# Optimization experiments

Measured on AMD Instinct MI355X. Metric: run time of the kernel, lower is better.

## Reference

```python
import jax, jax.numpy as jnp
import numpy as np

D = 64
H = 8


def setup_inputs() -> dict:
    key = jax.random.key(0)
    ks = jax.random.split(key, 6)
    b, l = 2, 4096
    scale = 1.0 / np.sqrt(D)
    x = jax.random.normal(ks[0], (b, l, D), dtype=jnp.float32)
    Wq = jax.random.normal(ks[1], (D, D * H), dtype=jnp.float32) * scale
    Wk = jax.random.normal(ks[2], (D, D * H), dtype=jnp.float32) * scale
    Wv = jax.random.normal(ks[3], (D, D * H), dtype=jnp.float32) * scale
    Wu = jax.random.normal(ks[4], (H * D, D), dtype=jnp.float32) * (1.0 / np.sqrt(H * D))
    bu = jax.random.normal(ks[5], (D,), dtype=jnp.float32) * 0.01
    return {"x": x, "Wq": Wq, "Wk": Wk, "Wv": Wv, "Wu": Wu, "bu": bu}


def reference(x, Wq, Wk, Wv, Wu, bu):
    b, l, d = x.shape
    h = H
    # per-head projections: each head uses FULL width d (as in the torch module)
    q = jnp.einsum('bld,de->ble', x, Wq).reshape(b, l, h, d)
    k = jnp.einsum('bld,de->ble', x, Wk).reshape(b, l, h, d)
    v = jnp.einsum('bld,de->ble', x, Wv).reshape(b, l, h, d)
    # scores [b,h,l,l] scaled by 1/sqrt(d)
    scores = jnp.einsum('blhd,bmhd->bhlm', q, k) / jnp.sqrt(jnp.asarray(d, x.dtype))
    w = jax.nn.softmax(scores, axis=-1)
    out = jnp.einsum('bhlm,bmhd->blhd', w, v).reshape(b, l, h * d)
    return out @ Wu + bu
```

## Files before the change

### kernel.cpp

```cpp
#include <hip/hip_runtime.h>
#include <hip/hip_bf16.h>
#include <stdint.h>

typedef float    f32x16 __attribute__((ext_vector_type(16)));
typedef float    f32x4  __attribute__((ext_vector_type(4)));
typedef __bf16   bf16x8 __attribute__((ext_vector_type(8)));
typedef uint32_t u32x4  __attribute__((ext_vector_type(4)));

#define WS_QG    0
#define WS_KG    8388608
#define WS_VTG   16777216
#define WS_ATTN  25165824
#define WS_WT    33554432
#define WS_WUT   33751040

__device__ __forceinline__ f32x16 zero16(){
  f32x16 z;
  #pragma unroll
  for (int i = 0; i < 16; ++i) z[i] = 0.0f;
  return z;
}

__device__ __forceinline__ uint16_t bf16b(float v){
  return __builtin_bit_cast(uint16_t, __float2bfloat16(v));
}

__device__ __forceinline__ uint32_t pk2(float a, float b){
  return (uint32_t)bf16b(a) | ((uint32_t)bf16b(b) << 16);
}

__device__ __forceinline__ void plswap(uint32_t &a, uint32_t &b){
  asm volatile("v_permlane32_swap_b32 %0, %1" : "+v"(a), "+v"(b));
}

__device__ __forceinline__ float sum16(const f32x16& s){
  float a0 = (s[0]+s[1]) + (s[2]+s[3]),   a1 = (s[4]+s[5]) + (s[6]+s[7]);
  float a2 = (s[8]+s[9]) + (s[10]+s[11]), a3 = (s[12]+s[13]) + (s[14]+s[15]);
  return (a0 + a1) + (a2 + a3);
}

__device__ __forceinline__ void bar_ws(){
  asm volatile("s_waitcnt lgkmcnt(0)" ::: "memory");
  __builtin_amdgcn_s_barrier();
  asm volatile("" ::: "memory");
}

__global__ void prep_w(const float* __restrict__ Wq, const float* __restrict__ Wk,
                       const float* __restrict__ Wv, const float* __restrict__ Wu,
                       char* __restrict__ ws){
  int tid = blockIdx.x * 256 + threadIdx.x;
  if (tid < 3*32768){
    int which = tid >> 15;
    int idx   = tid & 32767;
    int e = idx & 511, k = idx >> 9;
    const float* W = (which == 0) ? Wq : (which == 1 ? Wk : Wv);
    float v = W[k*512 + e];
    if (which == 0) v *= 0.18033688011112042f;
    ((uint16_t*)(ws + WS_WT))[which*32768 + e*64 + k] = bf16b(v);
  } else {
    int idx = tid - 3*32768;
    int c = idx & 63, e = idx >> 6;
    ((uint16_t*)(ws + WS_WUT))[c*512 + e] = bf16b(Wu[e*64 + c]);
  }
}

__global__ __launch_bounds__(256,2) void qkv_proj(const float* __restrict__ x,
                                                  char* __restrict__ ws){
  const int lane = threadIdx.x & 63;
  const int widx = threadIdx.x >> 6;
  const int x8 = blockIdx.x & 7;
  const int o  = blockIdx.x >> 3;
  const int rt = x8*32 + o/6;
  const int rem = (o%6)*4 + widx;
  const int mm = rem >> 3, cb = rem & 7;
  const int col  = lane & 31, hi = lane >> 5;

  __shared__ __align__(16) uint16_t tbuf[4][64*40];

  const uint16_t* Wt = (const uint16_t*)(ws + WS_WT) + mm*32768;

  bf16x8 af[4];
  {
    const float* xr = x + (size_t)(rt*32 + col)*64 + hi*8;
    #pragma unroll
    for (int ks = 0; ks < 4; ++ks){
      float4 a0 = *(const float4*)(xr + ks*16);
      float4 a1 = *(const float4*)(xr + ks*16 + 4);
      uint4 u;
      u.x = pk2(a0.x, a0.y); u.y = pk2(a0.z, a0.w);
      u.z = pk2(a1.x, a1.y); u.w = pk2(a1.z, a1.w);
      af[ks] = __builtin_bit_cast(bf16x8, u);
    }
  }

  f32x16 acc0 = zero16(), acc1 = zero16();
  {
    const uint16_t* w0p = Wt + (size_t)(cb*64 + col)*64 + hi*8;
    const uint16_t* w1p = w0p + 32*64;
    #pragma unroll
    for (int ks = 0; ks < 4; ++ks){
      bf16x8 b0 = *(const bf16x8*)(w0p + ks*16);
      bf16x8 b1 = *(const bf16x8*)(w1p + ks*16);
      acc0 = __builtin_amdgcn_mfma_f32_32x32x16_bf16(af[ks], b0, acc0, 0, 0, 0);
      acc1 = __builtin_amdgcn_mfma_f32_32x32x16_bf16(af[ks], b1, acc1, 0, 0, 0);
    }
  }

  uint16_t* Qg  = (uint16_t*)(ws + WS_QG);
  uint16_t* Kg  = (uint16_t*)(ws + WS_KG);
  uint16_t* Vtg = (uint16_t*)(ws + WS_VTG);
  if (mm == 2){
    uint16_t* tb = tbuf[widx];
    #pragma unroll
    for (int r = 0; r < 16; ++r){
      int tok = (r&3) + 8*(r>>2) + 4*hi;
      tb[col*40 + tok]        = bf16b(acc0[r]);
      tb[(col+32)*40 + tok]   = bf16b(acc1[r]);
    }
    int b    = (rt*32) >> 12;
    int ltok = (rt*32) & 4095;
    const int vrow = lane >> 2, ch = lane & 3;
    #pragma unroll
    for (int o2 = 0; o2 < 4; ++o2){
      int dv = o2*16 + vrow;
      uint4 u = *(const uint4*)(tb + dv*40 + ch*8);
      *(uint4*)(Vtg + ((size_t)((b*8 + cb)*64 + dv))*4096 + ltok + ch*8) = u;
    }
  } else {
    uint16_t* G = mm ? Kg : Qg;
    #pragma unroll
    for (int r = 0; r < 16; ++r){
      int row  = rt*32 + (r&3) + 8*(r>>2) + 4*hi;
      int b    = row >> 12, ltok = row & 4095;
      size_t base = (size_t)((b*8 + cb)*4096 + ltok)*64;
      G[base + col]      = bf16b(acc0[r]);
      G[base + col + 32] = bf16b(acc1[r]);
    }
  }
}

__global__ __launch_bounds__(256,1) void attn_fa(char* __restrict__ ws){
  const int lane = threadIdx.x & 63;
  const int wave = threadIdx.x >> 6;
  const int u   = blockIdx.x >> 3;
  const int bh  = (blockIdx.x & 7) + ((u >> 4) << 3);
  const int qt  = u & 15;
  const int col = lane & 31, hi = lane >> 5;
  const int kxor = (col & 7) << 4;

  const uint16_t* Qg  = (const uint16_t*)(ws + WS_QG)  + (size_t)bh*262144;
  const uint16_t* Kg  = (const uint16_t*)(ws + WS_KG)  + (size_t)bh*262144;
  const uint16_t* Vtg = (const uint16_t*)(ws + WS_VTG) + (size_t)bh*262144;
  uint16_t* attn = (uint16_t*)(ws + WS_ATTN);

  __shared__ __align__(16) char smem[33792];
  char* buf0 = smem;
  char* buf1 = smem + 16384;

  const int qbase = qt*256 + wave*64;

  bf16x8 qf0[4], qf1[4];
  {
    const uint16_t* qr0 = Qg + (size_t)(qbase + col)*64 + hi*8;
    const uint16_t* qr1 = qr0 + 32*64;
    #pragma unroll
    for (int ds = 0; ds < 4; ++ds){
      qf0[ds] = *(const bf16x8*)(qr0 + ds*16);
      qf1[ds] = *(const bf16x8*)(qr1 + ds*16);
    }
  }

  const int rr = lane >> 3, ch = lane & 7;
  const int kRow0 = wave*16 + rr;
  const uint16_t* kSrc = Kg  + (size_t)kRow0*64   + ch*8;
  const uint16_t* vSrc = Vtg + (size_t)kRow0*4096 + ch*8;
  const int sDst = kRow0*128 + ((ch*16) ^ (rr << 4));

  f32x16 ot00 = zero16(), ot01 = zero16(), ot10 = zero16(), ot11 = zero16();
  float rs0 = 0.0f, rs1 = 0.0f;

  u32x4 rK0, rK1, rV0, rV1;
  auto loadKV = [&](int t){
    const uint16_t* ks = kSrc + (size_t)t*4096;
    const uint16_t* vs = vSrc + t*64;
    rK0 = *(const u32x4*)(ks);
    rK1 = *(const u32x4*)(ks + 512);
    rV0 = *(const u32x4*)(vs);
    rV1 = *(const u32x4*)(vs + (size_t)8*4096);
  };
  auto writeKV = [&](char* buf){
    *(u32x4*)(buf + sDst)           = rK0;
    *(u32x4*)(buf + sDst + 1024)    = rK1;
    *(u32x4*)(buf + 8192 + sDst)        = rV0;
    *(u32x4*)(buf + 8192 + sDst + 1024) = rV1;
  };

  auto pack2 = [&](const f32x16& s, bf16x8& f0, bf16x8& f1){
    uint32_t w0 = pk2(s[0],  s[1]),  w1 = pk2(s[2],  s[3]);
    uint32_t w2 = pk2(s[4],  s[5]),  w3 = pk2(s[6],  s[7]);
    uint32_t w4 = pk2(s[8],  s[9]),  w5 = pk2(s[10], s[11]);
    uint32_t w6 = pk2(s[12], s[13]), w7 = pk2(s[14], s[15]);
    plswap(w0, w2); plswap(w1, w3); plswap(w4, w6); plswap(w5, w7);
    u32x4 u0; u0.x = w0; u0.y = w1; u0.z = w2; u0.w = w3;
    u32x4 u1; u1.x = w4; u1.y = w5; u1.z = w6; u1.w = w7;
    f0 = __builtin_bit_cast(bf16x8, u0);
    f1 = __builtin_bit_cast(bf16x8, u1);
  };

  auto compute = [&](const char* buf){
    const char* kb = buf;
    const char* vb = buf + 8192;
    bf16x8 pA[4], pB[4];
    #pragma unroll
    for (int ks2 = 0; ks2 < 2; ++ks2){
      f32x16 sA = zero16(), sB = zero16();
      __builtin_amdgcn_s_setprio(1);
      #pragma unroll
      for (int ds = 0; ds < 4; ++ds){
        bf16x8 kf = *(const bf16x8*)(kb + (ks2*32 + col)*128 + ((ds*32 + hi*16) ^ kxor));
        sA = __builtin_amdgcn_mfma_f32_32x32x16_bf16(kf, qf0[ds], sA, 0, 0, 0);
        sB = __builtin_amdgcn_mfma_f32_32x32x16_bf16(kf, qf1[ds], sB, 0, 0, 0);
      }
      __builtin_amdgcn_s_setprio(0);
      #pragma unroll
      for (int r = 0; r < 16; ++r) sA[r] = __builtin_amdgcn_exp2f(sA[r]);
      #pragma unroll
      for (int r = 0; r < 16; ++r) sB[r] = __builtin_amdgcn_exp2f(sB[r]);
      rs0 += sum16(sA);
      rs1 += sum16(sB);
      pack2(sA, pA[ks2*2], pA[ks2*2+1]);
      pack2(sB, pB[ks2*2], pB[ks2*2+1]);
    }
    __builtin_amdgcn_s_setprio(1);
    #pragma unroll
    for (int sl = 0; sl < 4; ++sl){
      bf16x8 vf0 = *(const bf16x8*)(vb + col*128 + ((sl*32 + hi*16) ^ kxor));
      ot00 = __builtin_amdgcn_mfma_f32_32x32x16_bf16(vf0, pA[sl], ot00, 0, 0, 0);
      ot01 = __builtin_amdgcn_mfma_f32_32x32x16_bf16(vf0, pB[sl], ot01, 0, 0, 0);
      bf16x8 vf1 = *(const bf16x8*)(vb + (32 + col)*128 + ((sl*32 + hi*16) ^ kxor));
      ot10 = __builtin_amdgcn_mfma_f32_32x32x16_bf16(vf1, pA[sl], ot10, 0, 0, 0);
      ot11 = __builtin_amdgcn_mfma_f32_32x32x16_bf16(vf1, pB[sl], ot11, 0, 0, 0);
    }
    __builtin_amdgcn_s_setprio(0);
  };

  loadKV(0);
  writeKV(buf0);
  loadKV(1);
  bar_ws();

  for (int t = 0; t < 64; ++t){
    char* cur = (t & 1) ? buf1 : buf0;
    char* nxt = (t & 1) ? buf0 : buf1;
    writeKV(nxt);
    loadKV((t+2 < 64) ? t+2 : 63);
    compute(cur);
    bar_ws();
  }

  rs0 += __shfl_xor(rs0, 32);
  rs1 += __shfl_xor(rs1, 32);
  float inv0 = 1.0f / rs0, inv1 = 1.0f / rs1;

  uint32_t* ow = (uint32_t*)(smem + wave*8448);
  #pragma unroll
  for (int od = 0; od < 2; ++od){
    #pragma unroll
    for (int j = 0; j < 8; ++j){
      int p = (j&1) + 4*(j>>1) + 2*hi + 16*od;
      const f32x16& a0 = od ? ot10 : ot00;
      const f32x16& a1 = od ? ot11 : ot01;
      ow[(col     )*33 + p] = pk2(a0[2*j]*inv0, a0[2*j+1]*inv0);
      ow[(col + 32)*33 + p] = pk2(a1[2*j]*inv1, a1[2*j+1]*inv1);
    }
  }
  {
    #pragma unroll
    for (int oo = 0; oo < 8; ++oo){
      int q = oo*8 + rr;
      u32x4 uu = *(const u32x4*)(ow + q*33 + ch*4);
      size_t row = (size_t)((bh >> 3)*4096 + qbase + q);
      *(u32x4*)(attn + row*512 + (bh & 7)*64 + ch*8) = uu;
    }
  }
}

__global__ __launch_bounds__(256) void out_proj(const char* __restrict__ ws,
                                                const float* __restrict__ bu,
                                                float* __restrict__ out){
  const int lane = threadIdx.x & 63;
  const int wave = blockIdx.x*4 + (threadIdx.x >> 6);
  const int mt = wave >> 2, cb = wave & 3;
  const int rc = lane & 15, kg = lane >> 4;

  const uint16_t* attn = (const uint16_t*)(ws + WS_ATTN);
  const uint16_t* Wut  = (const uint16_t*)(ws + WS_WUT);

  const uint16_t* ar = attn + (size_t)(mt*16 + rc)*512 + kg*8;
  const uint16_t* bp = Wut  + (size_t)(cb*16 + rc)*512 + kg*8;

  f32x4 acc = {0.0f, 0.0f, 0.0f, 0.0f};
  #pragma unroll
  for (int ks = 0; ks < 16; ++ks){
    bf16x8 af = *(const bf16x8*)(ar + ks*32);
    bf16x8 bf = *(const bf16x8*)(bp + ks*32);
    acc = __builtin_amdgcn_mfma_f32_16x16x32_bf16(af, bf, acc, 0, 0, 0);
  }
  float bias = bu[cb*16 + rc];
  #pragma unroll
  for (int r = 0; r < 4; ++r){
    int orow = mt*16 + kg*4 + r;
    out[(size_t)orow*64 + cb*16 + rc] = acc[r] + bias;
  }
}

extern "C" void kernel_launch(void* const* d_in, const int* in_sizes, int n_in,
                              void* d_out, int out_size, void* d_ws, size_t ws_size,
                              hipStream_t stream){
  const float* x  = (const float*)d_in[0];
  const float* Wq = (const float*)d_in[1];
  const float* Wk = (const float*)d_in[2];
  const float* Wv = (const float*)d_in[3];
  const float* Wu = (const float*)d_in[4];
  const float* bu = (const float*)d_in[5];
  char*  ws  = (char*)d_ws;
  float* out = (float*)d_out;

  prep_w  <<<dim3(512),  dim3(256), 0, stream>>>(Wq, Wk, Wv, Wu, ws);
  qkv_proj<<<dim3(1536), dim3(256), 0, stream>>>(x, ws);
  attn_fa <<<dim3(256),  dim3(256), 0, stream>>>(ws);
  out_proj<<<dim3(512),  dim3(256), 0, stream>>>(ws, bu, out);
}
```

Measured before the change: 197.4 us.

## Split attention KV range across wave pairs and stage Q/K stores through LDS

The attention kernel now launches twice as many blocks with 128 query rows each. The four waves split into two query halves times two KV halves, and the partial outputs and row sums are merged through shared memory before normalization. This is meant to raise occupancy and CU coverage (512 blocks, launch bounds 2) and to halve the serial KV loop per wave. The cost is doubled LDS per block and an extra reduction step. Separately, Q/K writes in the projection kernel are transposed through LDS so they become coalesced 16-byte stores instead of scattered 2-byte stores.

Measured after the change: 178.9 us. -9.3%, faster.

```diff
diff --git a/kernel.cpp b/kernel.cpp
--- a/kernel.cpp
+++ b/kernel.cpp
@@ -75,7 +75,7 @@
   const int mm = rem >> 3, cb = rem & 7;
   const int col  = lane & 31, hi = lane >> 5;
 
-  __shared__ __align__(16) uint16_t tbuf[4][64*40];
+  __shared__ __align__(16) uint16_t tbuf[4][2560];
 
   const uint16_t* Wt = (const uint16_t*)(ws + WS_WT) + mm*32768;
 
@@ -109,42 +109,49 @@
   uint16_t* Qg  = (uint16_t*)(ws + WS_QG);
   uint16_t* Kg  = (uint16_t*)(ws + WS_KG);
   uint16_t* Vtg = (uint16_t*)(ws + WS_VTG);
+  uint16_t* tb  = tbuf[widx];
+  const int b     = (rt*32) >> 12;
+  const int ltok0 = (rt*32) & 4095;
   if (mm == 2){
-    uint16_t* tb = tbuf[widx];
     #pragma unroll
     for (int r = 0; r < 16; ++r){
       int tok = (r&3) + 8*(r>>2) + 4*hi;
       tb[col*40 + tok]        = bf16b(acc0[r]);
       tb[(col+32)*40 + tok]   = bf16b(acc1[r]);
     }
-    int b    = (rt*32) >> 12;
-    int ltok = (rt*32) & 4095;
     const int vrow = lane >> 2, ch = lane & 3;
     #pragma unroll
     for (int o2 = 0; o2 < 4; ++o2){
       int dv = o2*16 + vrow;
-      uint4 u = *(const uint4*)(tb + dv*40 + ch*8);
-      *(uint4*)(Vtg + ((size_t)((b*8 + cb)*64 + dv))*4096 + ltok + ch*8) = u;
+      u32x4 u = *(const u32x4*)(tb + dv*40 + ch*8);
+      *(u32x4*)(Vtg + ((size_t)((b*8 + cb)*64 + dv))*4096 + ltok0 + ch*8) = u;
     }
   } else {
     uint16_t* G = mm ? Kg : Qg;
     #pragma unroll
     for (int r = 0; r < 16; ++r){
-      int row  = rt*32 + (r&3) + 8*(r>>2) + 4*hi;
-      int b    = row >> 12, ltok = row & 4095;
-      size_t base = (size_t)((b*8 + cb)*4096 + ltok)*64;
-      G[base + col]      = bf16b(acc0[r]);
-      G[base + col + 32] = bf16b(acc1[r]);
-    }
-  }
-}
-
-__global__ __launch_bounds__(256,1) void attn_fa(char* __restrict__ ws){
+      int tok = (r&3) + 8*(r>>2) + 4*hi;
+      tb[tok*72 + col]      = bf16b(acc0[r]);
+      tb[tok*72 + 32 + col] = bf16b(acc1[r]);
+    }
+    const int rr2 = lane >> 3, ch2 = lane & 7;
+    size_t base = (size_t)((b*8 + cb)*4096 + ltok0)*64;
+    #pragma unroll
+    for (int o2 = 0; o2 < 4; ++o2){
+      int tok = o2*8 + rr2;
+      u32x4 uu = *(const u32x4*)(tb + tok*72 + ch2*8);
+      *(u32x4*)(G + base + (size_t)tok*64 + ch2*8) = uu;
+    }
+  }
+}
+
+__global__ __launch_bounds__(256,2) void attn_fa(char* __restrict__ ws){
   const int lane = threadIdx.x & 63;
   const int wave = threadIdx.x >> 6;
+  const int qh = wave & 1, kvh = wave >> 1;
   const int u   = blockIdx.x >> 3;
-  const int bh  = (blockIdx.x & 7) + ((u >> 4) << 3);
-  const int qt  = u & 15;
+  const int bh  = (blockIdx.x & 7) + ((u >> 5) << 3);
+  const int qt  = u & 31;
   const int col = lane & 31, hi = lane >> 5;
   const int kxor = (col & 7) << 4;
 
@@ -153,11 +160,12 @@
   const uint16_t* Vtg = (const uint16_t*)(ws + WS_VTG) + (size_t)bh*262144;
   uint16_t* attn = (uint16_t*)(ws + WS_ATTN);
 
-  __shared__ __align__(16) char smem[33792];
-  char* buf0 = smem;
-  char* buf1 = smem + 16384;
-
-  const int qbase = qt*256 + wave*64;
+  __shared__ __align__(16) char smem[65536];
+  char* sbase = smem + kvh*32768;
+  char* buf0 = sbase;
+  char* buf1 = sbase + 16384;
+
+  const int qbase = qt*128 + qh*64;
 
   bf16x8 qf0[4], qf1[4];
   {
@@ -171,28 +179,28 @@
   }
 
   const int rr = lane >> 3, ch = lane & 7;
-  const int kRow0 = wave*16 + rr;
-  const uint16_t* kSrc = Kg  + (size_t)kRow0*64   + ch*8;
-  const uint16_t* vSrc = Vtg + (size_t)kRow0*4096 + ch*8;
-  const int sDst = kRow0*128 + ((ch*16) ^ (rr << 4));
+  const int srow = qh*8 + rr;
+  const uint16_t* kSrcB = Kg  + (size_t)(kvh*2048 + srow)*64 + ch*8;
+  const uint16_t* vSrcB = Vtg + (size_t)srow*4096 + kvh*2048 + ch*8;
+  const int sDstB = srow*128 + ((ch*16) ^ (rr << 4));
 
   f32x16 ot00 = zero16(), ot01 = zero16(), ot10 = zero16(), ot11 = zero16();
   float rs0 = 0.0f, rs1 = 0.0f;
 
-  u32x4 rK0, rK1, rV0, rV1;
+  u32x4 rK[4], rV[4];
   auto loadKV = [&](int t){
-    const uint16_t* ks = kSrc + (size_t)t*4096;
-    const uint16_t* vs = vSrc + t*64;
-    rK0 = *(const u32x4*)(ks);
-    rK1 = *(const u32x4*)(ks + 512);
-    rV0 = *(const u32x4*)(vs);
-    rV1 = *(const u32x4*)(vs + (size_t)8*4096);
+    const uint16_t* ks = kSrcB + (size_t)t*4096;
+    const uint16_t* vs = vSrcB + t*64;
+    #pragma unroll
+    for (int o2 = 0; o2 < 4; ++o2) rK[o2] = *(const u32x4*)(ks + o2*1024);
+    #pragma unroll
+    for (int o2 = 0; o2 < 4; ++o2) rV[o2] = *(const u32x4*)(vs + (size_t)o2*65536);
   };
   auto writeKV = [&](char* buf){
-    *(u32x4*)(buf + sDst)           = rK0;
-    *(u32x4*)(buf + sDst + 1024)    = rK1;
-    *(u32x4*)(buf + 8192 + sDst)        = rV0;
-    *(u32x4*)(buf + 8192 + sDst + 1024) = rV1;
+    #pragma unroll
+    for (int o2 = 0; o2 < 4; ++o2) *(u32x4*)(buf + sDstB + o2*2048) = rK[o2];
+    #pragma unroll
+    for (int o2 = 0; o2 < 4; ++o2) *(u32x4*)(buf + 8192 + sDstB + o2*2048) = rV[o2];
   };
 
   auto pack2 = [&](const f32x16& s, bf16x8& f0, bf16x8& f1){
@@ -249,38 +257,64 @@
   loadKV(1);
   bar_ws();
 
-  for (int t = 0; t < 64; ++t){
+  for (int t = 0; t < 32; ++t){
     char* cur = (t & 1) ? buf1 : buf0;
     char* nxt = (t & 1) ? buf0 : buf1;
     writeKV(nxt);
-    loadKV((t+2 < 64) ? t+2 : 63);
+    loadKV((t+2 < 32) ? t+2 : 31);
     compute(cur);
     bar_ws();
   }
 
-  rs0 += __shfl_xor(rs0, 32);
-  rs1 += __shfl_xor(rs1, 32);
-  float inv0 = 1.0f / rs0, inv1 = 1.0f / rs1;
-
-  uint32_t* ow = (uint32_t*)(smem + wave*8448);
-  #pragma unroll
-  for (int od = 0; od < 2; ++od){
-    #pragma unroll
-    for (int j = 0; j < 8; ++j){
-      int p = (j&1) + 4*(j>>1) + 2*hi + 16*od;
-      const f32x16& a0 = od ? ot10 : ot00;
-      const f32x16& a1 = od ? ot11 : ot01;
-      ow[(col     )*33 + p] = pk2(a0[2*j]*inv0, a0[2*j+1]*inv0);
-      ow[(col + 32)*33 + p] = pk2(a1[2*j]*inv1, a1[2*j+1]*inv1);
-    }
-  }
-  {
+  float* m = (float*)(smem + qh*17408) + lane*68;
+  if (kvh){
+    #pragma unroll
+    for (int j = 0; j < 4; ++j){
+      *(f32x4*)(m +      4*j) = f32x4{ot00[4*j], ot00[4*j+1], ot00[4*j+2], ot00[4*j+3]};
+      *(f32x4*)(m + 16 + 4*j) = f32x4{ot01[4*j], ot01[4*j+1], ot01[4*j+2], ot01[4*j+3]};
+      *(f32x4*)(m + 32 + 4*j) = f32x4{ot10[4*j], ot10[4*j+1], ot10[4*j+2], ot10[4*j+3]};
+      *(f32x4*)(m + 48 + 4*j) = f32x4{ot11[4*j], ot11[4*j+1], ot11[4*j+2], ot11[4*j+3]};
+    }
+    m[64] = rs0; m[65] = rs1;
+  }
+  bar_ws();
+  if (!kvh){
+    #pragma unroll
+    for (int j = 0; j < 4; ++j){
+      f32x4 v0 = *(const f32x4*)(m +      4*j);
+      f32x4 v1 = *(const f32x4*)(m + 16 + 4*j);
+      f32x4 v2 = *(const f32x4*)(m + 32 + 4*j);
+      f32x4 v3 = *(const f32x4*)(m + 48 + 4*j);
+      #pragma unroll
+      for (int e = 0; e < 4; ++e){
+        ot00[4*j+e] += v0[e]; ot01[4*j+e] += v1[e];
+        ot10[4*j+e] += v2[e]; ot11[4*j+e] += v3[e];
+      }
+    }
+    rs0 += m[64];  rs1 += m[65];
+    rs0 += __shfl_xor(rs0, 32);
+    rs1 += __shfl_xor(rs1, 32);
+    float inv0 = 1.0f / rs0, inv1 = 1.0f / rs1;
+
+    uint32_t* ow = (uint32_t*)(smem + 36864 + qh*8448);
+    #pragma unroll
+    for (int od = 0; od < 2; ++od){
+      #pragma unroll
+      for (int j = 0; j < 8; ++j){
+        int p = (j&1) + 4*(j>>1) + 2*hi + 16*od;
+        const f32x16& a0 = od ? ot10 : ot00;
+        const f32x16& a1 = od ? ot11 : ot01;
+        ow[(col     )*33 + p] = pk2(a0[2*j]*inv0, a0[2*j+1]*inv0);
+        ow[(col + 32)*33 + p] = pk2(a1[2*j]*inv1, a1[2*j+1]*inv1);
+      }
+    }
+    const int rrE = lane >> 3, chE = lane & 7;
     #pragma unroll
     for (int oo = 0; oo < 8; ++oo){
-      int q = oo*8 + rr;
-      u32x4 uu = *(const u32x4*)(ow + q*33 + ch*4);
+      int q = oo*8 + rrE;
+      u32x4 uu = *(const u32x4*)(ow + q*33 + chE*4);
       size_t row = (size_t)((bh >> 3)*4096 + qbase + q);
-      *(u32x4*)(attn + row*512 + (bh & 7)*64 + ch*8) = uu;
+      *(u32x4*)(attn + row*512 + (bh & 7)*64 + chE*8) = uu;
     }
   }
 }
@@ -328,6 +362,6 @@
 
   prep_w  <<<dim3(512),  dim3(256), 0, stream>>>(Wq, Wk, Wv, Wu, ws);
   qkv_proj<<<dim3(1536), dim3(256), 0, stream>>>(x, ws);
-  attn_fa <<<dim3(256),  dim3(256), 0, stream>>>(ws);
+  attn_fa <<<dim3(512),  dim3(256), 0, stream>>>(ws);
   out_proj<<<dim3(512),  dim3(256), 0, stream>>>(ws, bu, out);
 }
```
